# Optimization experiments

Measured on AMD Instinct MI355X. Metric: run time of the kernel, lower is better.

Reference implementation:

```python
import jax, jax.numpy as jnp
import numpy as np

R = 10  # num_relations
NUM_GRAPHS = 64


def rgcn_layer(x, W, root, b, src, dst, etype):
    # x: [N, Din], W: [R, Din, H], root: [Din, H], b: [H]
    N = x.shape[0]
    H = W.shape[-1]
    # per-relation transform of all nodes: [R, N, H]
    h_all = jnp.einsum('nd,rdh->rnh', x, W)
    # gather transformed source features per edge by its relation: [E, H]
    msg = h_all[etype, src]
    # mean-aggregate per (dst, relation) pair, then sum over relations (PyG RGCNConv semantics)
    key = dst * R + etype
    sums = jax.ops.segment_sum(msg, key, num_segments=N * R)  # [N*R, H]
    cnt = jax.ops.segment_sum(jnp.ones((etype.shape[0],), x.dtype), key, num_segments=N * R)
    agg = (sums.reshape(N, R, H) / jnp.clip(cnt.reshape(N, R, 1), 1.0, None)).sum(axis=1)
    return agg + x @ root + b


def setup_inputs() -> dict:
    key = jax.random.key(0)
    ks = jax.random.split(key, 12)
    N, E, DIN, H = 100000, 3200000, 128, 64
    x = jax.random.normal(ks[0], (N, DIN), dtype=jnp.float32)
    edge_index = jax.random.randint(ks[1], (2, E), 0, N, dtype=jnp.int64)
    edge_type = jax.random.randint(ks[2], (E,), 0, R, dtype=jnp.int64)
    batch = jnp.sort(jax.random.randint(ks[3], (N,), 0, NUM_GRAPHS, dtype=jnp.int64))
    s1 = 1.0 / np.sqrt(DIN)
    s2 = 1.0 / np.sqrt(H)
    W1 = jax.random.uniform(ks[4], (R, DIN, H), jnp.float32, -s1, s1)
    root1 = jax.random.uniform(ks[5], (DIN, H), jnp.float32, -s1, s1)
    b1 = jnp.zeros((H,), jnp.float32)
    W2 = jax.random.uniform(ks[6], (R, H, H), jnp.float32, -s2, s2)
    root2 = jax.random.uniform(ks[7], (H, H), jnp.float32, -s2, s2)
    b2 = jnp.zeros((H,), jnp.float32)
    cls_w = jax.random.uniform(ks[8], (H, 1), jnp.float32, -s2, s2)
    cls_b = jnp.zeros((1,), jnp.float32)
    return {"x": x, "edge_index": edge_index, "edge_type": edge_type, "batch": batch,
            "W1": W1, "root1": root1, "b1": b1, "W2": W2, "root2": root2, "b2": b2,
            "cls_w": cls_w, "cls_b": cls_b}


def reference(x, edge_index, edge_type, batch, W1, root1, b1, W2, root2, b2, cls_w, cls_b):
    src, dst = edge_index[0], edge_index[1]
    h = jax.nn.relu(rgcn_layer(x, W1, root1, b1, src, dst, edge_type))   # dropout = identity (eval)
    h = jax.nn.relu(rgcn_layer(h, W2, root2, b2, src, dst, edge_type))
    # global mean pool per graph
    sums = jax.ops.segment_sum(h, batch, num_segments=NUM_GRAPHS)        # [G, H]
    cnt = jax.ops.segment_sum(jnp.ones((h.shape[0],), h.dtype), batch, num_segments=NUM_GRAPHS)
    pooled = sums / jnp.clip(cnt[:, None], 1.0, None)
    out = pooled @ cls_w + cls_b                                          # [G, 1]
    return out.reshape(-1)
```

## Files before the change

kernel.cpp:

```cpp
#include <hip/hip_runtime.h>

#define R_REL 10
#define HD 64
#define BSH 8
#define KPB (256 * R_REL)
#define SORT_CAP 12288

typedef __attribute__((ext_vector_type(8))) short short8;
typedef __attribute__((ext_vector_type(4))) float floatx4;
typedef __attribute__((ext_vector_type(8))) unsigned short ushort8;

__device__ inline unsigned short f32_to_bf16_rne(float f) {
    unsigned int u = __float_as_uint(f);
    unsigned int r = (u + 0x7FFFu + ((u >> 16) & 1u)) >> 16;
    return (unsigned short)r;
}
__device__ inline float bf16_to_f32(unsigned short h) {
    return __uint_as_float(((unsigned int)h) << 16);
}
__device__ inline float bf16lo(unsigned int u) { return __uint_as_float(u << 16); }
__device__ inline float bf16hi(unsigned int u) { return __uint_as_float(u & 0xFFFF0000u); }

__global__ __launch_bounds__(256) void bhist_kernel(const int* __restrict__ dst,
                                                    int* __restrict__ bcnt, int E) {
    __shared__ int l[512];
    int t = threadIdx.x;
    l[t] = 0; l[t + 256] = 0;
    __syncthreads();
    int e0 = blockIdx.x * 4096;
    for (int i = t; i < 4096; i += 256) {
        int e = e0 + i;
        if (e < E) atomicAdd(&l[dst[e] >> BSH], 1);
    }
    __syncthreads();
    if (l[t]) atomicAdd(&bcnt[t], l[t]);
    if (l[t + 256]) atomicAdd(&bcnt[t + 256], l[t + 256]);
}

__global__ void bscan_kernel(const int* __restrict__ bcnt, int* __restrict__ boff,
                             int* __restrict__ gcursor, int NBK, int E) {
    int t = threadIdx.x;
    int v = (t < NBK) ? bcnt[t] : 0;
    __shared__ int tmp[512];
    tmp[t] = v;
    __syncthreads();
    for (int off = 1; off < 512; off <<= 1) {
        int u = (t >= off) ? tmp[t - off] : 0;
        __syncthreads();
        tmp[t] += u;
        __syncthreads();
    }
    int excl = tmp[t] - v;
    if (t < NBK) { boff[t] = excl; gcursor[t] = excl; }
    if (t == 0) boff[NBK] = E;
}

__global__ __launch_bounds__(256) void bscatter_kernel(const int* __restrict__ src,
                                                       const int* __restrict__ dst,
                                                       const int* __restrict__ et,
                                                       int* __restrict__ gcursor,
                                                       int2* __restrict__ staged, int E) {
    __shared__ int lcnt[512];
    __shared__ int lbase[512];
    int t = threadIdx.x;
    int e0 = blockIdx.x * 4096;
    lcnt[t] = 0; lcnt[t + 256] = 0;
    __syncthreads();
    for (int i = t; i < 4096; i += 256) {
        int e = e0 + i;
        if (e < E) atomicAdd(&lcnt[dst[e] >> BSH], 1);
    }
    __syncthreads();
    int c0 = lcnt[t], c1 = lcnt[t + 256];
    lbase[t]       = (c0 > 0) ? atomicAdd(&gcursor[t], c0) : 0;
    lbase[t + 256] = (c1 > 0) ? atomicAdd(&gcursor[t + 256], c1) : 0;
    lcnt[t] = 0; lcnt[t + 256] = 0;
    __syncthreads();
    for (int i = t; i < 4096; i += 256) {
        int e = e0 + i;
        if (e < E) {
            int dd = dst[e];
            int bk = dd >> BSH;
            int pos = lbase[bk] + atomicAdd(&lcnt[bk], 1);
            staged[pos] = make_int2(src[e], dd * R_REL + et[e]);
        }
    }
}

__global__ __launch_bounds__(256) void sortfill_kernel(const int2* __restrict__ staged,
                                                       const int* __restrict__ boff,
                                                       int* __restrict__ dcnt,
                                                       int2* __restrict__ edata,
                                                       int N, int Ntot) {
    __shared__ int hist[KPB];
    __shared__ float wkey[KPB];
    __shared__ int part[256];
    __shared__ int lsrc[SORT_CAP];
    __shared__ unsigned short lkey[SORT_CAP];
    int t = threadIdx.x, b = blockIdx.x;
    int s0 = boff[b], s1 = boff[b + 1];
    int keylo = b * KPB;
#pragma unroll
    for (int j = 0; j < KPB / 256; ++j) hist[t + j * 256] = 0;
    __syncthreads();
    for (int i = s0 + t; i < s1; i += 256)
        atomicAdd(&hist[staged[i].y - keylo], 1);
    __syncthreads();
    int base = t * (KPB / 256);
    int c[KPB / 256];
    int s = 0;
#pragma unroll
    for (int j = 0; j < KPB / 256; ++j) {
        c[j] = hist[base + j]; s += c[j];
        wkey[base + j] = 1.0f / fmaxf((float)c[j], 1.0f);
    }
    int dglob = b * 256 + t;
    if (dglob < Ntot) dcnt[dglob] = s;
    part[t] = s;
    __syncthreads();
    for (int off = 1; off < 256; off <<= 1) {
        int u = (t >= off) ? part[t - off] : 0;
        __syncthreads();
        part[t] += u;
        __syncthreads();
    }
    int run = part[t] - s;
#pragma unroll
    for (int j = 0; j < KPB / 256; ++j) { hist[base + j] = run; run += c[j]; }
    __syncthreads();
    for (int i = s0 + t; i < s1; i += 256) {
        int2 p = staged[i];
        int lk = p.y - keylo;
        int pos = atomicAdd(&hist[lk], 1);
        if (pos < SORT_CAP) { lsrc[pos] = p.x; lkey[pos] = (unsigned short)lk; }
        else {
            int rel = lk % R_REL;
            edata[s0 + pos] = make_int2(rel * N + p.x, __float_as_int(wkey[lk]));
        }
    }
    __syncthreads();
    int m = min(s1 - s0, SORT_CAP);
    for (int j = t; j < m; j += 256) {
        int lk = lkey[j];
        int rel = lk % R_REL;
        edata[s0 + j] = make_int2(rel * N + lsrc[j], __float_as_int(wkey[lk]));
    }
}

__global__ void scan1_kernel(const int* __restrict__ cnt, int* __restrict__ bsum, int M) {
    int b = blockIdx.x, tid = threadIdx.x;
    int base = b * 1024 + tid * 4;
    int s = 0;
#pragma unroll
    for (int j = 0; j < 4; ++j) { int i = base + j; if (i < M) s += cnt[i]; }
    for (int off = 32; off > 0; off >>= 1) s += __shfl_down(s, off);
    __shared__ int wsum[4];
    int lane = tid & 63, wid = tid >> 6;
    if (lane == 0) wsum[wid] = s;
    __syncthreads();
    if (tid == 0) bsum[b] = wsum[0] + wsum[1] + wsum[2] + wsum[3];
}

__global__ void scan2_kernel(const int* __restrict__ bsum, int* __restrict__ boff, int NB) {
    int tid = threadIdx.x;
    int lane = tid & 63, wid = tid >> 6;
    int v = (tid < NB) ? bsum[tid] : 0;
    int x = v;
    for (int off = 1; off < 64; off <<= 1) { int u = __shfl_up(x, off); if (lane >= off) x += u; }
    __shared__ int wsum[16];
    if (lane == 63) wsum[wid] = x;
    __syncthreads();
    int woff = 0;
    for (int w = 0; w < wid; ++w) woff += wsum[w];
    if (tid < NB) boff[tid] = x + woff - v;
}

__global__ void scan3_kernel(const int* __restrict__ cnt, const int* __restrict__ boff,
                             int* __restrict__ rowptr, int M) {
    int b = blockIdx.x, tid = threadIdx.x;
    int base = b * 1024 + tid * 4;
    int c[4]; int s = 0;
#pragma unroll
    for (int j = 0; j < 4; ++j) { int i = base + j; c[j] = (i < M) ? cnt[i] : 0; s += c[j]; }
    int lane = tid & 63, wid = tid >> 6;
    int x = s;
    for (int off = 1; off < 64; off <<= 1) { int u = __shfl_up(x, off); if (lane >= off) x += u; }
    __shared__ int wsum[4];
    if (lane == 63) wsum[wid] = x;
    __syncthreads();
    int woff = 0;
    for (int w = 0; w < wid; ++w) woff += wsum[w];
    int run = boff[b] + x + woff - s;
#pragma unroll
    for (int j = 0; j < 4; ++j) {
        int i = base + j;
        if (i < M) {
            rowptr[i] = run; run += c[j];
            if (i == M - 1) rowptr[M] = run;
        }
    }
}

__global__ void split_kernel(const float* __restrict__ src, unsigned short* __restrict__ hi,
                             unsigned short* __restrict__ lo, int n) {
    int i = blockIdx.x * 256 + threadIdx.x;
    if (i < n) {
        float v = src[i];
        unsigned short h = f32_to_bf16_rne(v);
        hi[i] = h;
        lo[i] = f32_to_bf16_rne(v - bf16_to_f32(h));
    }
}

__global__ void wsplit_kernel(const float* __restrict__ W, const float* __restrict__ root,
                              unsigned short* __restrict__ hi, unsigned short* __restrict__ lo,
                              int K) {
    int idx = blockIdx.x * 256 + threadIdx.x;
    int total = (R_REL + 1) * HD * K;
    if (idx >= total) return;
    int rel = idx / (HD * K);
    int rem = idx - rel * HD * K;
    int n = rem / K, k = rem - n * K;
    float v = (rel < R_REL) ? W[((size_t)rel * K + k) * HD + n] : root[(size_t)k * HD + n];
    unsigned short h = f32_to_bf16_rne(v);
    hi[idx] = h;
    lo[idx] = f32_to_bf16_rne(v - bf16_to_f32(h));
}

template <int K>
__global__ __launch_bounds__(256, 1) void gemm_mfma(const unsigned short* __restrict__ Xhi,
                                                    const unsigned short* __restrict__ Xlo,
                                                    const unsigned short* __restrict__ Wthi,
                                                    const unsigned short* __restrict__ Wtlo,
                                                    unsigned short* __restrict__ hout,
                                                    float* __restrict__ fout,
                                                    int N) {
    constexpr int LDK = K + 8;
    constexpr int NS = K / 32;
    __shared__ unsigned short xs_hi[64 * LDK];
    __shared__ unsigned short xs_lo[64 * LDK];
    const int tid = threadIdx.x;
    const int w = tid >> 6, lane = tid & 63;
    const int n0 = blockIdx.x * 64;
    constexpr int CH = K / 8;
    constexpr int RPI = 256 / CH;
#pragma unroll
    for (int it = 0; it < 64 / RPI; ++it) {
        int row = it * RPI + tid / CH;
        int ck = (tid & (CH - 1)) * 8;
        int node = n0 + row;
        ushort8 vh, vl;
#pragma unroll
        for (int q = 0; q < 8; ++q) { vh[q] = 0; vl[q] = 0; }
        if (node < N) {
            vh = *(const ushort8*)(Xhi + (size_t)node * K + ck);
            vl = *(const ushort8*)(Xlo + (size_t)node * K + ck);
        }
        *(ushort8*)&xs_hi[row * LDK + ck] = vh;
        *(ushort8*)&xs_lo[row * LDK + ck] = vl;
    }
    __syncthreads();
    const int quad = lane >> 4, l16 = lane & 15;
    const int colg = w * 16 + l16;
    short8 Ah[4][NS], Al[4][NS];
#pragma unroll
    for (int mt = 0; mt < 4; ++mt) {
#pragma unroll
        for (int s = 0; s < NS; ++s) {
            int ko = s * 32 + quad * 8;
            Ah[mt][s] = *(const short8*)&xs_hi[(mt * 16 + l16) * LDK + ko];
            Al[mt][s] = *(const short8*)&xs_lo[(mt * 16 + l16) * LDK + ko];
        }
    }
    __syncthreads();
    ((volatile unsigned short*)xs_hi)[tid] = 0;
    ((volatile unsigned short*)xs_lo)[tid] = 0;
#pragma unroll
    for (int c = 0; c <= R_REL; ++c) {
        const unsigned short* bh_base = Wthi + ((size_t)c * HD + colg) * K + quad * 8;
        const unsigned short* bl_base = Wtlo + ((size_t)c * HD + colg) * K + quad * 8;
        floatx4 zero = {0.f, 0.f, 0.f, 0.f};
        floatx4 acc[4];
#pragma unroll
        for (int mt = 0; mt < 4; ++mt) acc[mt] = zero;
#pragma unroll
        for (int s = 0; s < NS; ++s) {
            short8 bh = *(const short8*)(bh_base + s * 32);
            short8 bl = *(const short8*)(bl_base + s * 32);
#pragma unroll
            for (int mt = 0; mt < 4; ++mt) {
                acc[mt] = __builtin_amdgcn_mfma_f32_16x16x32_bf16(Ah[mt][s], bh, acc[mt], 0, 0, 0);
                acc[mt] = __builtin_amdgcn_mfma_f32_16x16x32_bf16(Al[mt][s], bh, acc[mt], 0, 0, 0);
                acc[mt] = __builtin_amdgcn_mfma_f32_16x16x32_bf16(Ah[mt][s], bl, acc[mt], 0, 0, 0);
            }
        }
#pragma unroll
        for (int mt = 0; mt < 4; ++mt) {
#pragma unroll
            for (int r = 0; r < 4; ++r) {
                int node = n0 + mt * 16 + quad * 4 + r;
                if (node < N) {
                    if (c < R_REL)
                        hout[(size_t)c * N * HD + (size_t)node * HD + colg] =
                            f32_to_bf16_rne(acc[mt][r]);
                    else
                        fout[(size_t)node * HD + colg] = acc[mt][r];
                }
            }
        }
    }
}

__global__ __launch_bounds__(256) void agg_kernel(const unsigned short* __restrict__ hc,
                                                  const int* __restrict__ rowptr,
                                                  const int2* __restrict__ edata,
                                                  float* __restrict__ acc, int N) {
    int gid = blockIdx.x * 256 + threadIdx.x;
    int d = gid >> 6;
    if (d >= N) return;
    int lane = threadIdx.x & 63;
    int quarter = lane >> 4, l16 = lane & 15;
    int e0 = rowptr[d], e1 = rowptr[d + 1];
    int ne = e1 - e0;
    if (ne == 0) return;
    float s0 = 0.f, s1 = 0.f, s2 = 0.f, s3 = 0.f;
    for (int rb = 0; rb < ne; rb += 64) {
        int nthis = min(64, ne - rb);
        int2 ed = make_int2(0, 0);
        if (lane < nthis) ed = edata[e0 + rb + lane];
        int off = ed.x << 6;
        float wv = __int_as_float(ed.y);
        for (int j = 0; j < nthis; j += 8) {
            int   oa = __shfl(off, j + quarter);
            float wa = __shfl(wv,  j + quarter);
            int   ob = __shfl(off, j + 4 + quarter);
            float wb = __shfl(wv,  j + 4 + quarter);
            uint2 da = *(const uint2*)(hc + oa + l16 * 4);
            uint2 db = *(const uint2*)(hc + ob + l16 * 4);
            s0 += wa * bf16lo(da.x); s1 += wa * bf16hi(da.x);
            s2 += wa * bf16lo(da.y); s3 += wa * bf16hi(da.y);
            s0 += wb * bf16lo(db.x); s1 += wb * bf16hi(db.x);
            s2 += wb * bf16lo(db.y); s3 += wb * bf16hi(db.y);
        }
    }
    s0 += __shfl_xor(s0, 16); s1 += __shfl_xor(s1, 16);
    s2 += __shfl_xor(s2, 16); s3 += __shfl_xor(s3, 16);
    s0 += __shfl_xor(s0, 32); s1 += __shfl_xor(s1, 32);
    s2 += __shfl_xor(s2, 32); s3 += __shfl_xor(s3, 32);
    if (lane < 16) {
        float4* ap = (float4*)(acc + (size_t)d * HD + l16 * 4);
        float4 a = *ap;
        a.x += s0; a.y += s1; a.z += s2; a.w += s3;
        *ap = a;
    }
}

__global__ void fin1_kernel(const float* __restrict__ acc, const float* __restrict__ bias,
                            unsigned short* __restrict__ hi, unsigned short* __restrict__ lo,
                            int NH) {
    int i = blockIdx.x * 256 + threadIdx.x;
    if (i < NH) {
        float v = fmaxf(acc[i] + bias[i & (HD - 1)], 0.f);
        unsigned short h = f32_to_bf16_rne(v);
        hi[i] = h;
        lo[i] = f32_to_bf16_rne(v - bf16_to_f32(h));
    }
}

__global__ __launch_bounds__(256) void pool_kernel(const float* __restrict__ acc,
                                                   const float* __restrict__ bias,
                                                   const int* __restrict__ batch,
                                                   float* __restrict__ pooled,
                                                   float* __restrict__ gcnt, int N) {
    int w = blockIdx.x * 4 + (threadIdx.x >> 6);
    int lane = threadIdx.x & 63;
    int base = w * 64;
    if (base >= N) return;
    int nn = min(64, N - base);
    float b = bias[lane];
    int g_l = (base + lane < N) ? batch[base + lane] : -1;
    int g_first = __shfl(g_l, 0);
    int g_last = __shfl(g_l, nn - 1);
    if (nn == 64 && g_first == g_last) {
        float p0 = 0.f, p1 = 0.f, p2 = 0.f, p3 = 0.f;
#pragma unroll
        for (int i = 0; i < 64; i += 4) {
            p0 += fmaxf(acc[(size_t)(base + i + 0) * HD + lane] + b, 0.f);
            p1 += fmaxf(acc[(size_t)(base + i + 1) * HD + lane] + b, 0.f);
            p2 += fmaxf(acc[(size_t)(base + i + 2) * HD + lane] + b, 0.f);
            p3 += fmaxf(acc[(size_t)(base + i + 3) * HD + lane] + b, 0.f);
        }
        atomicAdd(&pooled[g_first * HD + lane], (p0 + p1) + (p2 + p3));
        if (lane == 0) atomicAdd(&gcnt[g_first], 64.f);
    } else {
        int cur = g_first; float s = 0.f; int cnt = 0;
        for (int i = 0; i < nn; ++i) {
            int g = __shfl(g_l, i);
            if (g != cur) {
                atomicAdd(&pooled[cur * HD + lane], s);
                if (lane == 0) atomicAdd(&gcnt[cur], (float)cnt);
                cur = g; s = 0.f; cnt = 0;
            }
            s += fmaxf(acc[(size_t)(base + i) * HD + lane] + b, 0.f);
            cnt++;
        }
        atomicAdd(&pooled[cur * HD + lane], s);
        if (lane == 0) atomicAdd(&gcnt[cur], (float)cnt);
    }
}

__global__ void cls_kernel(const float* __restrict__ pooled, const float* __restrict__ gcnt,
                           const float* __restrict__ cls_w, const float* __restrict__ cls_b,
                           float* __restrict__ out) {
    int g = threadIdx.x;
    float invc = 1.0f / fmaxf(gcnt[g], 1.0f);
    float acc = 0.f;
    for (int j = 0; j < 64; ++j) acc += pooled[g * 64 + j] * cls_w[j];
    out[g] = acc * invc + cls_b[0];
}

extern "C" void kernel_launch(void* const* d_in, const int* in_sizes, int n_in,
                              void* d_out, int out_size, void* d_ws, size_t ws_size,
                              hipStream_t stream) {
    const float* x     = (const float*)d_in[0];
    const int*   eidx  = (const int*)d_in[1];
    const int*   et    = (const int*)d_in[2];
    const int*   batch = (const int*)d_in[3];
    const float* W1    = (const float*)d_in[4];
    const float* root1 = (const float*)d_in[5];
    const float* b1    = (const float*)d_in[6];
    const float* W2    = (const float*)d_in[7];
    const float* root2 = (const float*)d_in[8];
    const float* b2    = (const float*)d_in[9];
    const float* cls_w = (const float*)d_in[10];
    const float* cls_b = (const float*)d_in[11];

    const int N = in_sizes[3];
    const int E = in_sizes[2];
    const int NB = (N + 1023) / 1024;
    const int NBK = (N + (1 << BSH) - 1) >> BSH;
    const int* srcp = eidx;
    const int* dstp = eidx + E;

    char* ws = (char*)d_ws;
    size_t off = 0;
    auto alloc = [&](size_t bytes) -> void* {
        void* p = ws + off;
        off = (off + bytes + 255) & ~(size_t)255;
        return p;
    };
    unsigned short* Xhi  = (unsigned short*)alloc((size_t)N * 128 * 2);
    unsigned short* Xlo  = (unsigned short*)alloc((size_t)N * 128 * 2);
    float*          accb = (float*)alloc((size_t)N * HD * 4);
    unsigned short* Wt1hi = (unsigned short*)alloc((size_t)(R_REL + 1) * HD * 128 * 2);
    unsigned short* Wt1lo = (unsigned short*)alloc((size_t)(R_REL + 1) * HD * 128 * 2);
    unsigned short* Wt2hi = (unsigned short*)alloc((size_t)(R_REL + 1) * HD * HD * 2);
    unsigned short* Wt2lo = (unsigned short*)alloc((size_t)(R_REL + 1) * HD * HD * 2);
    int2*  edata  = (int2*)alloc((size_t)E * 8);
    int*   rowptr = (int*)alloc((size_t)(N + 1) * 4);
    int*   dcnt   = (int*)alloc((size_t)N * 4);
    int*   bsum   = (int*)alloc((size_t)NB * 4);
    int*   bofs   = (int*)alloc((size_t)NB * 4);
    int*   bcnt   = (int*)alloc(512 * 4);
    int*   bboff  = (int*)alloc(513 * 4);
    int*   gcur   = (int*)alloc(512 * 4);
    float* pooled = (float*)alloc((size_t)(64 * HD + 64) * 4);
    float* gcnt   = pooled + 64 * HD;
    unsigned short* h_chunk = (unsigned short*)alloc((size_t)R_REL * N * HD * 2);

    int2* staged = (int2*)Xhi;
    unsigned short* H1hi = Xhi;
    unsigned short* H1lo = Xlo;

    hipMemsetAsync(bcnt, 0, 512 * 4, stream);
    hipMemsetAsync(pooled, 0, (size_t)(64 * HD + 64) * 4, stream);

    int nchunks = (E + 4095) / 4096;
    bhist_kernel<<<nchunks, 256, 0, stream>>>(dstp, bcnt, E);
    bscan_kernel<<<1, 512, 0, stream>>>(bcnt, bboff, gcur, NBK, E);
    bscatter_kernel<<<nchunks, 256, 0, stream>>>(srcp, dstp, et, gcur, staged, E);
    sortfill_kernel<<<NBK, 256, 0, stream>>>(staged, bboff, dcnt, edata, N, N);
    scan1_kernel<<<NB, 256, 0, stream>>>(dcnt, bsum, N);
    scan2_kernel<<<1, 1024, 0, stream>>>(bsum, bofs, NB);
    scan3_kernel<<<NB, 256, 0, stream>>>(dcnt, bofs, rowptr, N);

    int NK = N * 128;
    split_kernel<<<(NK + 255) / 256, 256, 0, stream>>>(x, Xhi, Xlo, NK);
    int tw1 = (R_REL + 1) * HD * 128, tw2 = (R_REL + 1) * HD * HD;
    wsplit_kernel<<<(tw1 + 255) / 256, 256, 0, stream>>>(W1, root1, Wt1hi, Wt1lo, 128);
    wsplit_kernel<<<(tw2 + 255) / 256, 256, 0, stream>>>(W2, root2, Wt2hi, Wt2lo, HD);

    const int gemmBlocks = (N + 63) / 64;
    const int aggBlocks  = (int)(((size_t)N * 64 + 255) / 256);
    const int NH = N * HD;

    gemm_mfma<128><<<gemmBlocks, 256, 0, stream>>>(Xhi, Xlo, Wt1hi, Wt1lo, h_chunk, accb, N);
    agg_kernel<<<aggBlocks, 256, 0, stream>>>(h_chunk, rowptr, edata, accb, N);
    fin1_kernel<<<(NH + 255) / 256, 256, 0, stream>>>(accb, b1, H1hi, H1lo, NH);

    gemm_mfma<64><<<gemmBlocks, 256, 0, stream>>>(H1hi, H1lo, Wt2hi, Wt2lo, h_chunk, accb, N);
    agg_kernel<<<aggBlocks, 256, 0, stream>>>(h_chunk, rowptr, edata, accb, N);

    int poolWaves = (N + 63) / 64;
    pool_kernel<<<(poolWaves + 3) / 4, 256, 0, stream>>>(accb, b2, batch, pooled, gcnt, N);
    cls_kernel<<<1, 64, 0, stream>>>(pooled, gcnt, cls_w, cls_b, (float*)d_out);
}
```

Baseline: 663.7 us.

## Double-buffer weight fragments and defer output stores in MFMA GEMM

```diff
diff --git a/kernel.cpp b/kernel.cpp
--- a/kernel.cpp
+++ b/kernel.cpp
@@ -228,7 +228,7 @@
 }
 
 template <int K>
-__global__ __launch_bounds__(256, 1) void gemm_mfma(const unsigned short* __restrict__ Xhi,
+__global__ __launch_bounds__(256, 2) void gemm_mfma(const unsigned short* __restrict__ Xhi,
                                                     const unsigned short* __restrict__ Xlo,
                                                     const unsigned short* __restrict__ Wthi,
                                                     const unsigned short* __restrict__ Wtlo,
@@ -262,50 +262,89 @@
     __syncthreads();
     const int quad = lane >> 4, l16 = lane & 15;
     const int colg = w * 16 + l16;
-    short8 Ah[4][NS], Al[4][NS];
+    short8 Ah[4][NS];
 #pragma unroll
     for (int mt = 0; mt < 4; ++mt) {
 #pragma unroll
         for (int s = 0; s < NS; ++s) {
-            int ko = s * 32 + quad * 8;
-            Ah[mt][s] = *(const short8*)&xs_hi[(mt * 16 + l16) * LDK + ko];
-            Al[mt][s] = *(const short8*)&xs_lo[(mt * 16 + l16) * LDK + ko];
+            Ah[mt][s] = *(const short8*)&xs_hi[(mt * 16 + l16) * LDK + s * 32 + quad * 8];
         }
     }
     __syncthreads();
     ((volatile unsigned short*)xs_hi)[tid] = 0;
-    ((volatile unsigned short*)xs_lo)[tid] = 0;
+
+    const bool full = (n0 + 64 <= N);
+    const unsigned short* bh0 = Wthi + (size_t)colg * K + quad * 8;
+    const unsigned short* bl0 = Wtlo + (size_t)colg * K + quad * 8;
+    short8 Bh[2][NS], Bl[2][NS];
+#pragma unroll
+    for (int s = 0; s < NS; ++s) {
+        Bh[0][s] = *(const short8*)(bh0 + s * 32);
+        Bl[0][s] = *(const short8*)(bl0 + s * 32);
+    }
+    floatx4 acc[2][4];
+    const size_t NHD = (size_t)N * HD;
+    const size_t obase = (size_t)(n0 + quad * 4) * HD + colg;
+
 #pragma unroll
     for (int c = 0; c <= R_REL; ++c) {
-        const unsigned short* bh_base = Wthi + ((size_t)c * HD + colg) * K + quad * 8;
-        const unsigned short* bl_base = Wtlo + ((size_t)c * HD + colg) * K + quad * 8;
+        const int cur = c & 1, nxt = cur ^ 1;
+        if (c < R_REL) {
+            const unsigned short* bh = bh0 + (size_t)(c + 1) * HD * K;
+            const unsigned short* bl = bl0 + (size_t)(c + 1) * HD * K;
+#pragma unroll
+            for (int s = 0; s < NS; ++s) {
+                Bh[nxt][s] = *(const short8*)(bh + s * 32);
+                Bl[nxt][s] = *(const short8*)(bl + s * 32);
+            }
+        }
         floatx4 zero = {0.f, 0.f, 0.f, 0.f};
-        floatx4 acc[4];
-#pragma unroll
-        for (int mt = 0; mt < 4; ++mt) acc[mt] = zero;
+#pragma unroll
+        for (int mt = 0; mt < 4; ++mt) acc[cur][mt] = zero;
 #pragma unroll
         for (int s = 0; s < NS; ++s) {
-            short8 bh = *(const short8*)(bh_base + s * 32);
-            short8 bl = *(const short8*)(bl_base + s * 32);
 #pragma unroll
             for (int mt = 0; mt < 4; ++mt) {
-                acc[mt] = __builtin_amdgcn_mfma_f32_16x16x32_bf16(Ah[mt][s], bh, acc[mt], 0, 0, 0);
-                acc[mt] = __builtin_amdgcn_mfma_f32_16x16x32_bf16(Al[mt][s], bh, acc[mt], 0, 0, 0);
-                acc[mt] = __builtin_amdgcn_mfma_f32_16x16x32_bf16(Ah[mt][s], bl, acc[mt], 0, 0, 0);
+                short8 Al = *(const short8*)&xs_lo[(mt * 16 + l16) * LDK + s * 32 + quad * 8];
+                acc[cur][mt] = __builtin_amdgcn_mfma_f32_16x16x32_bf16(Ah[mt][s], Bh[cur][s], acc[cur][mt], 0, 0, 0);
+                acc[cur][mt] = __builtin_amdgcn_mfma_f32_16x16x32_bf16(Al,        Bh[cur][s], acc[cur][mt], 0, 0, 0);
+                acc[cur][mt] = __builtin_amdgcn_mfma_f32_16x16x32_bf16(Ah[mt][s], Bl[cur][s], acc[cur][mt], 0, 0, 0);
             }
         }
+        if (c > 0) {
+            const int rr = c - 1;
+            if (rr < R_REL) {
+                unsigned short* hp = hout + (size_t)rr * NHD + obase;
+#pragma unroll
+                for (int mt = 0; mt < 4; ++mt) {
+#pragma unroll
+                    for (int r = 0; r < 4; ++r) {
+                        if (full || (n0 + mt * 16 + quad * 4 + r < N))
+                            hp[(size_t)(mt * 16 + r) * HD] = f32_to_bf16_rne(acc[nxt][mt][r]);
+                    }
+                }
+            } else {
+                float* fp = fout + obase;
+#pragma unroll
+                for (int mt = 0; mt < 4; ++mt) {
+#pragma unroll
+                    for (int r = 0; r < 4; ++r) {
+                        if (full || (n0 + mt * 16 + quad * 4 + r < N))
+                            fp[(size_t)(mt * 16 + r) * HD] = acc[nxt][mt][r];
+                    }
+                }
+            }
+        }
+    }
+    {
+        const int cur = R_REL & 1;
+        float* fp = fout + obase;
 #pragma unroll
         for (int mt = 0; mt < 4; ++mt) {
 #pragma unroll
             for (int r = 0; r < 4; ++r) {
-                int node = n0 + mt * 16 + quad * 4 + r;
-                if (node < N) {
-                    if (c < R_REL)
-                        hout[(size_t)c * N * HD + (size_t)node * HD + colg] =
-                            f32_to_bf16_rne(acc[mt][r]);
-                    else
-                        fout[(size_t)node * HD + colg] = acc[mt][r];
-                }
+                if (full || (n0 + mt * 16 + quad * 4 + r < N))
+                    fp[(size_t)(mt * 16 + r) * HD] = acc[cur][mt][r];
             }
         }
     }
```

New measurement: 646.5 us. 2.6% less time.

## Restructure MFMA GEMM to stage swizzled weight tiles in LDS with double buffering

Applied to the files above, without the earlier changes.

```diff
diff --git a/kernel.cpp b/kernel.cpp
--- a/kernel.cpp
+++ b/kernel.cpp
@@ -20,6 +20,12 @@
 }
 __device__ inline float bf16lo(unsigned int u) { return __uint_as_float(u << 16); }
 __device__ inline float bf16hi(unsigned int u) { return __uint_as_float(u & 0xFFFF0000u); }
+
+__device__ __forceinline__ void gload_lds16(const unsigned short* g, unsigned short* l) {
+    __builtin_amdgcn_global_load_lds(
+        (const __attribute__((address_space(1))) unsigned int*)g,
+        (__attribute__((address_space(3))) unsigned int*)l, 16, 0, 0);
+}
 
 __global__ __launch_bounds__(256) void bhist_kernel(const int* __restrict__ dst,
                                                     int* __restrict__ bcnt, int E) {
@@ -223,91 +229,104 @@
     int n = rem / K, k = rem - n * K;
     float v = (rel < R_REL) ? W[((size_t)rel * K + k) * HD + n] : root[(size_t)k * HD + n];
     unsigned short h = f32_to_bf16_rne(v);
-    hi[idx] = h;
-    lo[idx] = f32_to_bf16_rne(v - bf16_to_f32(h));
+    int ks = k ^ ((n & 7) << 3);
+    int widx = rel * HD * K + n * K + ks;
+    hi[widx] = h;
+    lo[widx] = f32_to_bf16_rne(v - bf16_to_f32(h));
 }
 
 template <int K>
-__global__ __launch_bounds__(256, 1) void gemm_mfma(const unsigned short* __restrict__ Xhi,
-                                                    const unsigned short* __restrict__ Xlo,
-                                                    const unsigned short* __restrict__ Wthi,
-                                                    const unsigned short* __restrict__ Wtlo,
-                                                    unsigned short* __restrict__ hout,
-                                                    float* __restrict__ fout,
-                                                    int N) {
-    constexpr int LDK = K + 8;
+__global__ __launch_bounds__(512, 4)
+void gemm_mfma(const unsigned short* __restrict__ Xhi,
+               const unsigned short* __restrict__ Xlo,
+               const unsigned short* __restrict__ Wthi,
+               const unsigned short* __restrict__ Wtlo,
+               unsigned short* __restrict__ hout,
+               float* __restrict__ fout, int N) {
     constexpr int NS = K / 32;
-    __shared__ unsigned short xs_hi[64 * LDK];
-    __shared__ unsigned short xs_lo[64 * LDK];
+    constexpr int TILE_SH = HD * K;
+    constexpr int TILEB = TILE_SH * 2;
+    constexpr int HALFC = K / 8;
+    __shared__ unsigned short wlds[4 * TILE_SH];
     const int tid = threadIdx.x;
     const int w = tid >> 6, lane = tid & 63;
-    const int n0 = blockIdx.x * 64;
-    constexpr int CH = K / 8;
-    constexpr int RPI = 256 / CH;
-#pragma unroll
-    for (int it = 0; it < 64 / RPI; ++it) {
-        int row = it * RPI + tid / CH;
-        int ck = (tid & (CH - 1)) * 8;
-        int node = n0 + row;
-        ushort8 vh, vl;
-#pragma unroll
-        for (int q = 0; q < 8; ++q) { vh[q] = 0; vl[q] = 0; }
-        if (node < N) {
-            vh = *(const ushort8*)(Xhi + (size_t)node * K + ck);
-            vl = *(const ushort8*)(Xlo + (size_t)node * K + ck);
-        }
-        *(ushort8*)&xs_hi[row * LDK + ck] = vh;
-        *(ushort8*)&xs_lo[row * LDK + ck] = vl;
-    }
-    __syncthreads();
     const int quad = lane >> 4, l16 = lane & 15;
-    const int colg = w * 16 + l16;
-    short8 Ah[4][NS], Al[4][NS];
-#pragma unroll
-    for (int mt = 0; mt < 4; ++mt) {
+    const int n0 = blockIdx.x * 128;
+    const int node = n0 + w * 16 + l16;
+    const bool valid = node < N;
+
+    short8 Xh[NS], Xl[NS];
+#pragma unroll
+    for (int s = 0; s < NS; ++s) {
+        short8 z;
+#pragma unroll
+        for (int q = 0; q < 8; ++q) z[q] = 0;
+        Xh[s] = z; Xl[s] = z;
+        if (valid) {
+            Xh[s] = *(const short8*)(Xhi + (size_t)node * K + s * 32 + quad * 8);
+            Xl[s] = *(const short8*)(Xlo + (size_t)node * K + s * 32 + quad * 8);
+        }
+    }
+
+    auto stage = [&](int rel, int b) {
+        const unsigned short* hsrc = Wthi + (size_t)rel * TILE_SH;
+        const unsigned short* lsrc = Wtlo + (size_t)rel * TILE_SH;
+        unsigned short* dst0 = wlds + b * 2 * TILE_SH;
+#pragma unroll
+        for (int j = 0; j < NS; ++j) {
+            int q = j * 8 + w;
+            const unsigned short* src = (q < HALFC) ? (hsrc + q * 512)
+                                                    : (lsrc + (q - HALFC) * 512);
+            gload_lds16(src + lane * 8, dst0 + q * 512);
+        }
+    };
+
+    stage(0, 0);
+    __syncthreads();
+
+    const int swzb = (l16 & 7) << 4;
+    const size_t NHD = (size_t)N * HD;
+
+#pragma unroll
+    for (int c = 0; c <= R_REL; ++c) {
+        const int cur = c & 1;
+        if (c < R_REL) stage(c + 1, cur ^ 1);
+        const char* wb = (const char*)(wlds + cur * 2 * TILE_SH);
+        floatx4 acc[4];
+#pragma unroll
+        for (int mt = 0; mt < 4; ++mt) { floatx4 z = {0.f, 0.f, 0.f, 0.f}; acc[mt] = z; }
 #pragma unroll
         for (int s = 0; s < NS; ++s) {
-            int ko = s * 32 + quad * 8;
-            Ah[mt][s] = *(const short8*)&xs_hi[(mt * 16 + l16) * LDK + ko];
-            Al[mt][s] = *(const short8*)&xs_lo[(mt * 16 + l16) * LDK + ko];
-        }
-    }
-    __syncthreads();
-    ((volatile unsigned short*)xs_hi)[tid] = 0;
-    ((volatile unsigned short*)xs_lo)[tid] = 0;
-#pragma unroll
-    for (int c = 0; c <= R_REL; ++c) {
-        const unsigned short* bh_base = Wthi + ((size_t)c * HD + colg) * K + quad * 8;
-        const unsigned short* bl_base = Wtlo + ((size_t)c * HD + colg) * K + quad * 8;
-        floatx4 zero = {0.f, 0.f, 0.f, 0.f};
-        floatx4 acc[4];
-#pragma unroll
-        for (int mt = 0; mt < 4; ++mt) acc[mt] = zero;
-#pragma unroll
-        for (int s = 0; s < NS; ++s) {
-            short8 bh = *(const short8*)(bh_base + s * 32);
-            short8 bl = *(const short8*)(bl_base + s * 32);
+            const int koffb = ((s * 32 + quad * 8) * 2) ^ swzb;
 #pragma unroll
             for (int mt = 0; mt < 4; ++mt) {
-                acc[mt] = __builtin_amdgcn_mfma_f32_16x16x32_bf16(Ah[mt][s], bh, acc[mt], 0, 0, 0);
-                acc[mt] = __builtin_amdgcn_mfma_f32_16x16x32_bf16(Al[mt][s], bh, acc[mt], 0, 0, 0);
-                acc[mt] = __builtin_amdgcn_mfma_f32_16x16x32_bf16(Ah[mt][s], bl, acc[mt], 0, 0, 0);
+                const int rowb = (mt * 16 + l16) * (K * 2);
+                short8 Wh = *(const short8*)(wb + rowb + koffb);
+                short8 Wl = *(const short8*)(wb + TILEB + rowb + koffb);
+                acc[mt] = __builtin_amdgcn_mfma_f32_16x16x32_bf16(Wh, Xh[s], acc[mt], 0, 0, 0);
+                acc[mt] = __builtin_amdgcn_mfma_f32_16x16x32_bf16(Wh, Xl[s], acc[mt], 0, 0, 0);
+                acc[mt] = __builtin_amdgcn_mfma_f32_16x16x32_bf16(Wl, Xh[s], acc[mt], 0, 0, 0);
             }
         }
-#pragma unroll
-        for (int mt = 0; mt < 4; ++mt) {
-#pragma unroll
-            for (int r = 0; r < 4; ++r) {
-                int node = n0 + mt * 16 + quad * 4 + r;
-                if (node < N) {
-                    if (c < R_REL)
-                        hout[(size_t)c * N * HD + (size_t)node * HD + colg] =
-                            f32_to_bf16_rne(acc[mt][r]);
-                    else
-                        fout[(size_t)node * HD + colg] = acc[mt][r];
+        if (valid) {
+            if (c < R_REL) {
+                unsigned short* hp = hout + (size_t)c * NHD + (size_t)node * HD + quad * 4;
+#pragma unroll
+                for (int mt = 0; mt < 4; ++mt) {
+                    unsigned int d0 = (unsigned int)f32_to_bf16_rne(acc[mt][0]) |
+                                      ((unsigned int)f32_to_bf16_rne(acc[mt][1]) << 16);
+                    unsigned int d1 = (unsigned int)f32_to_bf16_rne(acc[mt][2]) |
+                                      ((unsigned int)f32_to_bf16_rne(acc[mt][3]) << 16);
+                    *(uint2*)(hp + mt * 16) = make_uint2(d0, d1);
                 }
+            } else {
+                float* fp = fout + (size_t)node * HD + quad * 4;
+#pragma unroll
+                for (int mt = 0; mt < 4; ++mt)
+                    *(floatx4*)(fp + mt * 16) = acc[mt];
             }
         }
+        __syncthreads();
     }
 }
 
@@ -490,15 +509,15 @@
     wsplit_kernel<<<(tw1 + 255) / 256, 256, 0, stream>>>(W1, root1, Wt1hi, Wt1lo, 128);
     wsplit_kernel<<<(tw2 + 255) / 256, 256, 0, stream>>>(W2, root2, Wt2hi, Wt2lo, HD);
 
-    const int gemmBlocks = (N + 63) / 64;
+    const int gemmBlocks = (N + 127) / 128;
     const int aggBlocks  = (int)(((size_t)N * 64 + 255) / 256);
     const int NH = N * HD;
 
-    gemm_mfma<128><<<gemmBlocks, 256, 0, stream>>>(Xhi, Xlo, Wt1hi, Wt1lo, h_chunk, accb, N);
+    gemm_mfma<128><<<gemmBlocks, 512, 0, stream>>>(Xhi, Xlo, Wt1hi, Wt1lo, h_chunk, accb, N);
     agg_kernel<<<aggBlocks, 256, 0, stream>>>(h_chunk, rowptr, edata, accb, N);
     fin1_kernel<<<(NH + 255) / 256, 256, 0, stream>>>(accb, b1, H1hi, H1lo, NH);
 
-    gemm_mfma<64><<<gemmBlocks, 256, 0, stream>>>(H1hi, H1lo, Wt2hi, Wt2lo, h_chunk, accb, N);
+    gemm_mfma<64><<<gemmBlocks, 512, 0, stream>>>(H1hi, H1lo, Wt2hi, Wt2lo, h_chunk, accb, N);
     agg_kernel<<<aggBlocks, 256, 0, stream>>>(h_chunk, rowptr, edata, accb, N);
 
     int poolWaves = (N + 63) / 64;
```

Result: faster. 631.3 us (-4.9%).
